# Kernel tuning notes

Hardware: AMD Instinct MI355X
Metric: run time of the kernel (lower is better)

Reference implementation:

```python
import jax, jax.numpy as jnp
import numpy as np

NUM_NODES = 4
D = 1024            # hidden dim and dims of s_0, s_1; initial_input_dims = [D, D, 2D]
NUM_OPS = 5         # candidate ops per MixedLayer: linear, relu, tanh, sigmoid, leaky_relu(0.2)
NUM_LAYERS = 18     # sum_{i<4} (i+3)
BATCH = 4096

_ACTS = [
    lambda h: h,
    jax.nn.relu,
    jnp.tanh,
    jax.nn.sigmoid,
    lambda h: jax.nn.leaky_relu(h, 0.2),
]

def setup_inputs() -> dict:
    key = jax.random.key(0)
    ks = jax.random.split(key, 7)
    s_0 = jax.random.normal(ks[0], (BATCH, D), jnp.float32)
    s_1 = jax.random.normal(ks[1], (BATCH, D), jnp.float32)
    genotype = jax.random.uniform(ks[2], (NUM_LAYERS, NUM_OPS), jnp.float32)
    genotype = genotype / genotype.sum(-1, keepdims=True)  # softmax-like arch weights
    scale = 1.0 / np.sqrt(D)
    # 14 layers take a D-dim input; 4 layers (the cat(s_0,s_1) edge of each node) take 2D
    Ws = jax.random.normal(ks[3], (14, NUM_OPS, D, D), jnp.float32) * scale
    Wb = jax.random.normal(ks[4], (4, NUM_OPS, 2 * D, D), jnp.float32) * (scale / np.sqrt(2.0))
    bs = jax.random.normal(ks[5], (NUM_LAYERS, NUM_OPS, D), jnp.float32) * 0.01
    return {"s_0": s_0, "s_1": s_1, "genotype": genotype, "Ws": Ws, "Wb": Wb, "bs": bs}

def _mixed(x, W, b, w):
    # x: [B, in], W: [K, in, D], b: [K, D], w: [K]
    h = jnp.einsum('bi,kio->kbo', x, W) + b[:, None, :]
    out = 0.0
    for k, act in enumerate(_ACTS):
        out = out + w[k] * act(h[k])
    return out

def reference(s_0, s_1, genotype, Ws, Wb, bs):
    states = [s_0, s_1, jnp.concatenate([s_0, s_1], axis=-1)]
    offset, si, bi = 0, 0, 0
    for i in range(NUM_NODES):
        s = 0.0
        for j, cur in enumerate(states):
            l = offset + j
            if j == 2:  # edge from cat(s_0, s_1): input dim 2D
                W = Wb[bi]; bi += 1
            else:
                W = Ws[si]; si += 1
            s = s + _mixed(cur, W, bs[l], genotype[l])
        offset += len(states)
        states.append(s)
    return states[-1]
```

## Files before the change

kernel.cpp:

```cpp
#include <hip/hip_runtime.h>
#include <hip/hip_bf16.h>
#include <cstdint>
#include <cstddef>

typedef __attribute__((ext_vector_type(8))) short bf16x8;
typedef __attribute__((ext_vector_type(4))) float f32x4;

#define DEV __device__ __forceinline__

DEV unsigned short f2bf(float f) {
  unsigned int u = __float_as_uint(f);
  return (unsigned short)((u + 0x7fffu + ((u >> 16) & 1u)) >> 16);
}

DEV void gl_lds16(const unsigned short* g, unsigned short* l) {
  __builtin_amdgcn_global_load_lds(
      (__attribute__((address_space(1))) const void*)g,
      (__attribute__((address_space(3))) void*)l, 16, 0, 0);
}

__global__ __launch_bounds__(256) void cvt_kernel(const float* __restrict__ src,
                                                  unsigned short* __restrict__ dst) {
  size_t i = (size_t)blockIdx.x * 256 + threadIdx.x;
  float4 v = ((const float4*)src)[i];
  ushort4 o;
  o.x = f2bf(v.x); o.y = f2bf(v.y); o.z = f2bf(v.z); o.w = f2bf(v.w);
  ((ushort4*)dst)[i] = o;
}

__global__ __launch_bounds__(256) void zero_kernel(float* __restrict__ p) {
  size_t i = (size_t)blockIdx.x * 256 + threadIdx.x;
  ((float4*)p)[i] = make_float4(0.f, 0.f, 0.f, 0.f);
}

__global__ __launch_bounds__(256) void cvtzero_kernel(float* __restrict__ s,
                                                      unsigned short* __restrict__ dst) {
  size_t i = (size_t)blockIdx.x * 256 + threadIdx.x;
  float4 v = ((float4*)s)[i];
  ushort4 o;
  o.x = f2bf(v.x); o.y = f2bf(v.y); o.z = f2bf(v.z); o.w = f2bf(v.w);
  ((ushort4*)dst)[i] = o;
  ((float4*)s)[i] = make_float4(0.f, 0.f, 0.f, 0.f);
}

__global__ __launch_bounds__(256) void transpose_kernel(const float* __restrict__ src,
                                                        unsigned short* __restrict__ dst,
                                                        int K) {
  __shared__ float tile[64][68];
  const int t = threadIdx.x;
  const int tpm = (K >> 6) * 16;
  const int mat = blockIdx.x / tpm;
  const int r = blockIdx.x % tpm;
  const int tk = r >> 4;
  const int tn = r & 15;
  const size_t sbase = (size_t)mat * K * 1024 + (size_t)tk * 64 * 1024 + (size_t)tn * 64;
#pragma unroll
  for (int p = 0; p < 4; ++p) {
    int row = p * 16 + (t >> 4);
    int c4 = (t & 15) * 4;
    float4 v = *(const float4*)&src[sbase + (size_t)row * 1024 + c4];
    *(float4*)&tile[row][c4] = v;
  }
  __syncthreads();
  const size_t dbase = (size_t)mat * 1024 * K + (size_t)tn * 64 * K + (size_t)tk * 64;
#pragma unroll
  for (int p = 0; p < 4; ++p) {
    int n = p * 16 + (t >> 4);
    int k4 = (t & 15) * 4;
    ushort4 o;
    o.x = f2bf(tile[k4 + 0][n]);
    o.y = f2bf(tile[k4 + 1][n]);
    o.z = f2bf(tile[k4 + 2][n]);
    o.w = f2bf(tile[k4 + 3][n]);
    *(ushort4*)&dst[dbase + (size_t)n * K + k4] = o;
  }
}

struct EdgeCfg {
  const unsigned short* xlo;
  const unsigned short* xhi;
  const unsigned short* wt;
  int inlen;
  int l;
};
struct NodeArgs {
  EdgeCfg e[6];
  int nedges;
};

__global__ __launch_bounds__(256) void node_gemm(NodeArgs na,
                                                 const float* __restrict__ genotype,
                                                 const float* __restrict__ bs,
                                                 float* __restrict__ sout) {
  __shared__ unsigned short As[128 * 32];
  __shared__ unsigned short Bs[128 * 32];

  const int t = threadIdx.x;
  const int lane = t & 63;
  const int w = t >> 6;
  const int wm = (w & 1) * 64;
  const int wn = (w >> 1) * 64;
  const int bn = blockIdx.x * 128;
  const int bm = blockIdx.y * 128;
  const int kop = blockIdx.z;
  const int l15 = lane & 15;
  const int l16 = lane >> 4;

  const int srow = t >> 2;
  const int scol = (t & 3) * 8;

  f32x4 sacc[4][4];
#pragma unroll
  for (int mi = 0; mi < 4; ++mi)
#pragma unroll
    for (int ni = 0; ni < 4; ++ni) sacc[mi][ni] = (f32x4){0.f, 0.f, 0.f, 0.f};

  for (int e = 0; e < na.nedges; ++e) {
    const int inlen = na.e[e].inlen;
    const unsigned short* xlo = na.e[e].xlo;
    const unsigned short* xhi = na.e[e].xhi;
    const unsigned short* wtk = na.e[e].wt + (size_t)kop * inlen * 1024;
    const int l = na.e[e].l;
    const int nk = inlen >> 5;

    f32x4 hacc[4][4];
#pragma unroll
    for (int mi = 0; mi < 4; ++mi)
#pragma unroll
      for (int ni = 0; ni < 4; ++ni) hacc[mi][ni] = (f32x4){0.f, 0.f, 0.f, 0.f};

    for (int kt = 0; kt < nk; ++kt) {
      const int k0 = kt << 5;
      __syncthreads();
      const unsigned short* ax = (k0 < 1024) ? xlo : xhi;
      const int ak = k0 & 1023;
      gl_lds16(ax + (size_t)(bm + srow) * 1024 + ak + scol, As + t * 8);
      gl_lds16(ax + (size_t)(bm + 64 + srow) * 1024 + ak + scol, As + 2048 + t * 8);
      const unsigned short* wr = wtk + (size_t)(bn + srow) * inlen + k0 + scol;
      gl_lds16(wr, Bs + t * 8);
      gl_lds16(wr + (size_t)64 * inlen, Bs + 2048 + t * 8);
      __syncthreads();

      bf16x8 af[4], bfr[4];
#pragma unroll
      for (int mi = 0; mi < 4; ++mi)
        af[mi] = *(const bf16x8*)&As[(wm + mi * 16 + l15) * 32 + l16 * 8];
#pragma unroll
      for (int ni = 0; ni < 4; ++ni)
        bfr[ni] = *(const bf16x8*)&Bs[(wn + ni * 16 + l15) * 32 + l16 * 8];
#pragma unroll
      for (int mi = 0; mi < 4; ++mi)
#pragma unroll
        for (int ni = 0; ni < 4; ++ni)
          hacc[mi][ni] = __builtin_amdgcn_mfma_f32_16x16x32_bf16(af[mi], bfr[ni],
                                                                 hacc[mi][ni], 0, 0, 0);
    }

    const float wlk = genotype[l * 5 + kop];
    const float* bv = bs + ((size_t)l * 5 + kop) * 1024;
#pragma unroll
    for (int ni = 0; ni < 4; ++ni) {
      const float bias = bv[bn + wn + ni * 16 + l15];
#pragma unroll
      for (int mi = 0; mi < 4; ++mi)
#pragma unroll
        for (int i = 0; i < 4; ++i) {
          float h = hacc[mi][ni][i] + bias;
          float a;
          if (kop == 0) a = h;
          else if (kop == 1) a = fmaxf(h, 0.f);
          else if (kop == 2) a = 1.f - 2.f / (__expf(2.f * h) + 1.f);
          else if (kop == 3) a = 1.f / (1.f + __expf(-h));
          else a = (h > 0.f) ? h : 0.2f * h;
          sacc[mi][ni][i] += wlk * a;
        }
    }
  }

#pragma unroll
  for (int mi = 0; mi < 4; ++mi)
#pragma unroll
    for (int ni = 0; ni < 4; ++ni)
#pragma unroll
      for (int i = 0; i < 4; ++i) {
        const int row = bm + wm + mi * 16 + l16 * 4 + i;
        const int col = bn + wn + ni * 16 + l15;
        unsafeAtomicAdd(&sout[(size_t)row * 1024 + col], sacc[mi][ni][i]);
      }
}

extern "C" void kernel_launch(void* const* d_in, const int* in_sizes, int n_in,
                              void* d_out, int out_size, void* d_ws, size_t ws_size,
                              hipStream_t stream) {
  const float* s0 = (const float*)d_in[0];
  const float* s1 = (const float*)d_in[1];
  const float* geno = (const float*)d_in[2];
  const float* Ws = (const float*)d_in[3];
  const float* Wb = (const float*)d_in[4];
  const float* bs = (const float*)d_in[5];

  unsigned short* WsT = (unsigned short*)d_ws;
  unsigned short* WbT = WsT + 70ull * 1024 * 1024;
  unsigned short* S0 = WbT + 20ull * 2048 * 1024;
  unsigned short* S1 = S0 + 4096ull * 1024;
  unsigned short* T0 = S1 + 4096ull * 1024;
  unsigned short* T1 = T0 + 4096ull * 1024;
  unsigned short* T2 = T1 + 4096ull * 1024;
  float* S = (float*)(T2 + 4096ull * 1024);

  cvt_kernel<<<4096, 256, 0, stream>>>(s0, S0);
  cvt_kernel<<<4096, 256, 0, stream>>>(s1, S1);
  zero_kernel<<<4096, 256, 0, stream>>>(S);
  zero_kernel<<<4096, 256, 0, stream>>>((float*)d_out);
  transpose_kernel<<<70 * 256, 256, 0, stream>>>(Ws, WsT, 1024);
  transpose_kernel<<<20 * 512, 256, 0, stream>>>(Wb, WbT, 2048);

  auto SE = [&](const unsigned short* x, int si, int l) {
    EdgeCfg c;
    c.xlo = x; c.xhi = x;
    c.wt = WsT + (size_t)si * 5 * 1024 * 1024;
    c.inlen = 1024; c.l = l;
    return c;
  };
  auto BE = [&](int bi, int l) {
    EdgeCfg c;
    c.xlo = S0; c.xhi = S1;
    c.wt = WbT + (size_t)bi * 5 * 2048 * 1024;
    c.inlen = 2048; c.l = l;
    return c;
  };

  dim3 grid(8, 32, 5);
  {
    NodeArgs a{}; a.nedges = 3;
    a.e[0] = SE(S0, 0, 0); a.e[1] = SE(S1, 1, 1); a.e[2] = BE(0, 2);
    node_gemm<<<grid, 256, 0, stream>>>(a, geno, bs, S);
    cvtzero_kernel<<<4096, 256, 0, stream>>>(S, T0);
  }
  {
    NodeArgs a{}; a.nedges = 4;
    a.e[0] = SE(S0, 2, 3); a.e[1] = SE(S1, 3, 4); a.e[2] = BE(1, 5); a.e[3] = SE(T0, 4, 6);
    node_gemm<<<grid, 256, 0, stream>>>(a, geno, bs, S);
    cvtzero_kernel<<<4096, 256, 0, stream>>>(S, T1);
  }
  {
    NodeArgs a{}; a.nedges = 5;
    a.e[0] = SE(S0, 5, 7); a.e[1] = SE(S1, 6, 8); a.e[2] = BE(2, 9);
    a.e[3] = SE(T0, 7, 10); a.e[4] = SE(T1, 8, 11);
    node_gemm<<<grid, 256, 0, stream>>>(a, geno, bs, S);
    cvtzero_kernel<<<4096, 256, 0, stream>>>(S, T2);
  }
  {
    NodeArgs a{}; a.nedges = 6;
    a.e[0] = SE(S0, 9, 12); a.e[1] = SE(S1, 10, 13); a.e[2] = BE(3, 14);
    a.e[3] = SE(T0, 11, 15); a.e[4] = SE(T1, 12, 16); a.e[5] = SE(T2, 13, 17);
    node_gemm<<<grid, 256, 0, stream>>>(a, geno, bs, (float*)d_out);
  }
}
```

Baseline: 2.841 ms.

## Double-buffer LDS tiles, split 2D edges into segments, swizzle LDS layout

The GEMM main loop now uses two LDS buffers, so the global-to-LDS loads for the next K-tile are issued before computing on the current one. This removes one of the two barriers per tile and hides load latency. The 2D-input edges are split into two 1024-wide segments whose weights are re-laid out with a uniform 1024 row stride, so every segment runs a fixed 32-tile loop and the next segment's first tile is prefetched across boundaries. The LDS layout is also changed to an 8-row-interleaved arrangement, apparently to reduce bank conflicts on fragment reads. Launch bounds request two blocks per CU, which may pressure registers since hacc and sacc both stay live.

```diff
diff --git a/kernel.cpp b/kernel.cpp
--- a/kernel.cpp
+++ b/kernel.cpp
@@ -62,7 +62,9 @@
     *(float4*)&tile[row][c4] = v;
   }
   __syncthreads();
-  const size_t dbase = (size_t)mat * 1024 * K + (size_t)tn * 64 * K + (size_t)tk * 64;
+  const int kbase = tk * 64;
+  const size_t dbase = (size_t)mat * 1024 * K + (size_t)(kbase >> 10) * 1024 * 1024 +
+                       (size_t)tn * 64 * 1024 + (size_t)(kbase & 1023);
 #pragma unroll
   for (int p = 0; p < 4; ++p) {
     int n = p * 16 + (t >> 4);
@@ -72,28 +74,27 @@
     o.y = f2bf(tile[k4 + 1][n]);
     o.z = f2bf(tile[k4 + 2][n]);
     o.w = f2bf(tile[k4 + 3][n]);
-    *(ushort4*)&dst[dbase + (size_t)n * K + k4] = o;
-  }
-}
-
-struct EdgeCfg {
-  const unsigned short* xlo;
-  const unsigned short* xhi;
-  const unsigned short* wt;
-  int inlen;
+    *(ushort4*)&dst[dbase + (size_t)n * 1024 + k4] = o;
+  }
+}
+
+struct SegCfg {
+  const unsigned short* x;
+  const unsigned short* w;
+  size_t wops;
   int l;
+  int last;
 };
 struct NodeArgs {
-  EdgeCfg e[6];
-  int nedges;
+  SegCfg s[7];
+  int nseg;
 };
 
-__global__ __launch_bounds__(256) void node_gemm(NodeArgs na,
-                                                 const float* __restrict__ genotype,
-                                                 const float* __restrict__ bs,
-                                                 float* __restrict__ sout) {
-  __shared__ unsigned short As[128 * 32];
-  __shared__ unsigned short Bs[128 * 32];
+__global__ __launch_bounds__(256, 2) void node_gemm(NodeArgs na,
+                                                    const float* __restrict__ genotype,
+                                                    const float* __restrict__ bs,
+                                                    float* __restrict__ sout) {
+  __shared__ unsigned short lds[16384];
 
   const int t = threadIdx.x;
   const int lane = t & 63;
@@ -106,56 +107,61 @@
   const int l15 = lane & 15;
   const int l16 = lane >> 4;
 
-  const int srow = t >> 2;
-  const int scol = (t & 3) * 8;
+  const int srow = ((t >> 5) << 3) | (t & 7);
+  const int schunk = (t >> 3) & 3;
+  const size_t aoffg = (size_t)(bm + srow) * 1024 + schunk * 8;
+  const size_t boffg = (size_t)(bn + srow) * 1024 + schunk * 8;
+
+  unsigned short* dA0 = lds + t * 8;
+  unsigned short* dB0 = lds + 4096 + t * 8;
+  unsigned short* dA1 = lds + 8192 + t * 8;
+  unsigned short* dB1 = lds + 12288 + t * 8;
+
+  int aof[4], bof[4];
+#pragma unroll
+  for (int mi = 0; mi < 4; ++mi) {
+    int r = wm + mi * 16 + l15;
+    aof[mi] = (r >> 3) * 256 + l16 * 64 + (r & 7) * 8;
+  }
+#pragma unroll
+  for (int ni = 0; ni < 4; ++ni) {
+    int r = wn + ni * 16 + l15;
+    bof[ni] = (r >> 3) * 256 + l16 * 64 + (r & 7) * 8;
+  }
 
   f32x4 sacc[4][4];
+  f32x4 hacc[4][4];
 #pragma unroll
   for (int mi = 0; mi < 4; ++mi)
 #pragma unroll
-    for (int ni = 0; ni < 4; ++ni) sacc[mi][ni] = (f32x4){0.f, 0.f, 0.f, 0.f};
-
-  for (int e = 0; e < na.nedges; ++e) {
-    const int inlen = na.e[e].inlen;
-    const unsigned short* xlo = na.e[e].xlo;
-    const unsigned short* xhi = na.e[e].xhi;
-    const unsigned short* wtk = na.e[e].wt + (size_t)kop * inlen * 1024;
-    const int l = na.e[e].l;
-    const int nk = inlen >> 5;
-
-    f32x4 hacc[4][4];
+    for (int ni = 0; ni < 4; ++ni) {
+      sacc[mi][ni] = (f32x4){0.f, 0.f, 0.f, 0.f};
+      hacc[mi][ni] = (f32x4){0.f, 0.f, 0.f, 0.f};
+    }
+
+  auto stage = [&](const unsigned short* pa, const unsigned short* pb,
+                   unsigned short* da, unsigned short* db) {
+    gl_lds16(pa, da);
+    gl_lds16(pa + 64 * 1024, da + 2048);
+    gl_lds16(pb, db);
+    gl_lds16(pb + 64 * 1024, db + 2048);
+  };
+
+  auto compute = [&](const unsigned short* Ab, const unsigned short* Bb) {
+    bf16x8 af[4], bfr[4];
+#pragma unroll
+    for (int mi = 0; mi < 4; ++mi) af[mi] = *(const bf16x8*)&Ab[aof[mi]];
+#pragma unroll
+    for (int ni = 0; ni < 4; ++ni) bfr[ni] = *(const bf16x8*)&Bb[bof[ni]];
 #pragma unroll
     for (int mi = 0; mi < 4; ++mi)
 #pragma unroll
-      for (int ni = 0; ni < 4; ++ni) hacc[mi][ni] = (f32x4){0.f, 0.f, 0.f, 0.f};
-
-    for (int kt = 0; kt < nk; ++kt) {
-      const int k0 = kt << 5;
-      __syncthreads();
-      const unsigned short* ax = (k0 < 1024) ? xlo : xhi;
-      const int ak = k0 & 1023;
-      gl_lds16(ax + (size_t)(bm + srow) * 1024 + ak + scol, As + t * 8);
-      gl_lds16(ax + (size_t)(bm + 64 + srow) * 1024 + ak + scol, As + 2048 + t * 8);
-      const unsigned short* wr = wtk + (size_t)(bn + srow) * inlen + k0 + scol;
-      gl_lds16(wr, Bs + t * 8);
-      gl_lds16(wr + (size_t)64 * inlen, Bs + 2048 + t * 8);
-      __syncthreads();
-
-      bf16x8 af[4], bfr[4];
-#pragma unroll
-      for (int mi = 0; mi < 4; ++mi)
-        af[mi] = *(const bf16x8*)&As[(wm + mi * 16 + l15) * 32 + l16 * 8];
-#pragma unroll
       for (int ni = 0; ni < 4; ++ni)
-        bfr[ni] = *(const bf16x8*)&Bs[(wn + ni * 16 + l15) * 32 + l16 * 8];
-#pragma unroll
-      for (int mi = 0; mi < 4; ++mi)
-#pragma unroll
-        for (int ni = 0; ni < 4; ++ni)
-          hacc[mi][ni] = __builtin_amdgcn_mfma_f32_16x16x32_bf16(af[mi], bfr[ni],
-                                                                 hacc[mi][ni], 0, 0, 0);
-    }
-
+        hacc[mi][ni] = __builtin_amdgcn_mfma_f32_16x16x32_bf16(af[mi], bfr[ni],
+                                                               hacc[mi][ni], 0, 0, 0);
+  };
+
+  auto epilogue = [&](int l) {
     const float wlk = genotype[l * 5 + kop];
     const float* bv = bs + ((size_t)l * 5 + kop) * 1024;
 #pragma unroll
@@ -173,8 +179,42 @@
           else if (kop == 3) a = 1.f / (1.f + __expf(-h));
           else a = (h > 0.f) ? h : 0.2f * h;
           sacc[mi][ni][i] += wlk * a;
+          hacc[mi][ni][i] = 0.f;
         }
     }
+  };
+
+  const unsigned short* pa = na.s[0].x + aoffg;
+  const unsigned short* pb = na.s[0].w + (size_t)kop * na.s[0].wops + boffg;
+  int cl = na.s[0].l, clast = na.s[0].last;
+  stage(pa, pb, dA0, dB0);
+  __syncthreads();
+
+  for (int e = 0; e < na.nseg; ++e) {
+#pragma unroll 1
+    for (int kt2 = 0; kt2 < 15; ++kt2) {
+      stage(pa + (2 * kt2 + 1) * 32, pb + (2 * kt2 + 1) * 32, dA1, dB1);
+      compute(lds, lds + 4096);
+      __syncthreads();
+      stage(pa + (2 * kt2 + 2) * 32, pb + (2 * kt2 + 2) * 32, dA0, dB0);
+      compute(lds + 8192, lds + 12288);
+      __syncthreads();
+    }
+    stage(pa + 31 * 32, pb + 31 * 32, dA1, dB1);
+    compute(lds, lds + 4096);
+    __syncthreads();
+    if (e + 1 < na.nseg) {
+      pa = na.s[e + 1].x + aoffg;
+      pb = na.s[e + 1].w + (size_t)kop * na.s[e + 1].wops + boffg;
+      stage(pa, pb, dA0, dB0);
+    }
+    compute(lds + 8192, lds + 12288);
+    if (clast) epilogue(cl);
+    if (e + 1 < na.nseg) {
+      cl = na.s[e + 1].l;
+      clast = na.s[e + 1].last;
+    }
+    __syncthreads();
   }
 
 #pragma unroll
@@ -215,45 +255,52 @@
   transpose_kernel<<<70 * 256, 256, 0, stream>>>(Ws, WsT, 1024);
   transpose_kernel<<<20 * 512, 256, 0, stream>>>(Wb, WbT, 2048);
 
-  auto SE = [&](const unsigned short* x, int si, int l) {
-    EdgeCfg c;
-    c.xlo = x; c.xhi = x;
-    c.wt = WsT + (size_t)si * 5 * 1024 * 1024;
-    c.inlen = 1024; c.l = l;
+  auto SS = [&](const unsigned short* x, int si, int l) {
+    SegCfg c;
+    c.x = x;
+    c.w = WsT + (size_t)si * 5 * 1024 * 1024;
+    c.wops = (size_t)1024 * 1024;
+    c.l = l; c.last = 1;
     return c;
   };
-  auto BE = [&](int bi, int l) {
-    EdgeCfg c;
-    c.xlo = S0; c.xhi = S1;
-    c.wt = WbT + (size_t)bi * 5 * 2048 * 1024;
-    c.inlen = 2048; c.l = l;
+  auto BH = [&](int bi, int half, int l) {
+    SegCfg c;
+    c.x = half ? S1 : S0;
+    c.w = WbT + (size_t)bi * 5 * 2048 * 1024 + (size_t)half * 1024 * 1024;
+    c.wops = (size_t)2048 * 1024;
+    c.l = l; c.last = half;
     return c;
   };
 
   dim3 grid(8, 32, 5);
   {
-    NodeArgs a{}; a.nedges = 3;
-    a.e[0] = SE(S0, 0, 0); a.e[1] = SE(S1, 1, 1); a.e[2] = BE(0, 2);
+    NodeArgs a{}; a.nseg = 4;
+    a.s[0] = SS(S0, 0, 0); a.s[1] = SS(S1, 1, 1);
+    a.s[2] = BH(0, 0, 2); a.s[3] = BH(0, 1, 2);
     node_gemm<<<grid, 256, 0, stream>>>(a, geno, bs, S);
     cvtzero_kernel<<<4096, 256, 0, stream>>>(S, T0);
   }
   {
-    NodeArgs a{}; a.nedges = 4;
-    a.e[0] = SE(S0, 2, 3); a.e[1] = SE(S1, 3, 4); a.e[2] = BE(1, 5); a.e[3] = SE(T0, 4, 6);
+    NodeArgs a{}; a.nseg = 5;
+    a.s[0] = SS(S0, 2, 3); a.s[1] = SS(S1, 3, 4);
+    a.s[2] = BH(1, 0, 5); a.s[3] = BH(1, 1, 5);
+    a.s[4] = SS(T0, 4, 6);
     node_gemm<<<grid, 256, 0, stream>>>(a, geno, bs, S);
     cvtzero_kernel<<<4096, 256, 0, stream>>>(S, T1);
   }
   {
-    NodeArgs a{}; a.nedges = 5;
-    a.e[0] = SE(S0, 5, 7); a.e[1] = SE(S1, 6, 8); a.e[2] = BE(2, 9);
-    a.e[3] = SE(T0, 7, 10); a.e[4] = SE(T1, 8, 11);
+    NodeArgs a{}; a.nseg = 6;
+    a.s[0] = SS(S0, 5, 7); a.s[1] = SS(S1, 6, 8);
+    a.s[2] = BH(2, 0, 9); a.s[3] = BH(2, 1, 9);
+    a.s[4] = SS(T0, 7, 10); a.s[5] = SS(T1, 8, 11);
     node_gemm<<<grid, 256, 0, stream>>>(a, geno, bs, S);
     cvtzero_kernel<<<4096, 256, 0, stream>>>(S, T2);
   }
   {
-    NodeArgs a{}; a.nedges = 6;
-    a.e[0] = SE(S0, 9, 12); a.e[1] = SE(S1, 10, 13); a.e[2] = BE(3, 14);
-    a.e[3] = SE(T0, 11, 15); a.e[4] = SE(T1, 12, 16); a.e[5] = SE(T2, 13, 17);
+    NodeArgs a{}; a.nseg = 7;
+    a.s[0] = SS(S0, 9, 12); a.s[1] = SS(S1, 10, 13);
+    a.s[2] = BH(3, 0, 14); a.s[3] = BH(3, 1, 14);
+    a.s[4] = SS(T0, 11, 15); a.s[5] = SS(T1, 12, 16); a.s[6] = SS(T2, 13, 17);
     node_gemm<<<grid, 256, 0, stream>>>(a, geno, bs, (float*)d_out);
   }
 }
```

Result: no change. 2.826 ms (-0.5%).
